# Performance work log

Measured on AMD Instinct MI355X. Metric: run time of the kernel, lower is better.

Reference implementation:

```python
import jax, jax.numpy as jnp
import numpy as np

B, S, D, K = 16, 4096, 64, 4096

def setup_inputs() -> dict:
    key = jax.random.key(0)
    k1, k2 = jax.random.split(key)
    z = jax.random.normal(k1, (B, S, D), dtype=jnp.float32)
    # codebook initialized uniform(-1/K, 1/K) as in the torch module
    emb = jax.random.uniform(k2, (K, D), dtype=jnp.float32, minval=-1.0 / K, maxval=1.0 / K)
    return {"z": z, "emb": emb}

def reference(z, emb):
    Dm = emb.shape[1]
    flat_z = z.reshape(-1, Dm)                     # [N, D]
    # squared L2 distances to every codebook entry: [N, K]
    dist = (jnp.sum(flat_z * flat_z, axis=1, keepdims=True)
            + jnp.sum(emb * emb, axis=1)
            - 2.0 * flat_z @ emb.T)
    encoding_indices = jnp.argmin(dist, axis=1)    # [N]
    # one-hot @ emb is mathematically a gather; use the direct gather
    quantized = emb[encoding_indices].reshape(z.shape)
    quantized_st = z + jax.lax.stop_gradient(quantized - z)
    e_latent_loss = jnp.mean((jax.lax.stop_gradient(quantized) - z) ** 2)
    q_latent_loss = jnp.mean((quantized - jax.lax.stop_gradient(z)) ** 2)
    vq_loss = e_latent_loss + q_latent_loss
    return quantized_st, encoding_indices.reshape(z.shape[:-1]), vq_loss
```

## Files before the change

kernel.cpp:

```cpp
#include <hip/hip_runtime.h>

#define NTOK 65536
#define DDIM 64
#define KCB  4096
#define MB   64
#define NTILES 256
#define TPW  64
#define LCAP 6144
#define WWIN 5.0e-4f
#define IDXOFF  (NTOK * DDIM)
#define LOSSOFF (NTOK * DDIM + NTOK)
#define ZPAD 68

typedef __bf16 bf16x8 __attribute__((ext_vector_type(8)));
typedef float  f32x4  __attribute__((ext_vector_type(4)));

__device__ __forceinline__ float opaque(float x) { asm volatile("" : "+v"(x)); return x; }

__device__ __forceinline__ float np_sumsq64(const float* __restrict__ v) {
    float r[8];
#pragma unroll
    for (int j = 0; j < 8; ++j) r[j] = opaque(v[j] * v[j]);
#pragma unroll
    for (int i = 1; i < 8; ++i)
#pragma unroll
        for (int j = 0; j < 8; ++j) r[j] += opaque(v[8 * i + j] * v[8 * i + j]);
    return ((r[0] + r[1]) + (r[2] + r[3])) + ((r[4] + r[5]) + (r[6] + r[7]));
}

__device__ __forceinline__ unsigned short bf16rne(float x) {
    unsigned u = __float_as_uint(x);
    return (unsigned short)((u + 0x7fffu + ((u >> 16) & 1u)) >> 16);
}

__global__ void k_prep(const float* __restrict__ emb, float* __restrict__ e2,
                       uint4* __restrict__ pfh, double* __restrict__ lossacc) {
    int k = blockIdx.x * blockDim.x + threadIdx.x;
    if (k == 0) *lossacc = 0.0;
    if (k >= KCB) return;
    float row[DDIM];
    const float4* r4 = (const float4*)(emb + (size_t)k * DDIM);
#pragma unroll
    for (int i = 0; i < DDIM / 4; ++i) {
        float4 v = r4[i];
        row[4*i+0] = v.x; row[4*i+1] = v.y; row[4*i+2] = v.z; row[4*i+3] = v.w;
    }
    e2[k] = np_sumsq64(row);
    const int tile = k >> 4, rr = k & 15;
#pragma unroll
    for (int q = 0; q < 4; ++q) {
#pragma unroll
        for (int kh = 0; kh < 2; ++kh) {
            union { uint4 v; unsigned short s[8]; } th;
#pragma unroll
            for (int j = 0; j < 8; ++j) th.s[j] = bf16rne(row[q*8 + kh*32 + j]);
            pfh[(size_t)tile * 128 + kh * 64 + q * 16 + rr] = th.v;
        }
    }
}

__global__ __launch_bounds__(256, 4)
void k_vq(const float* __restrict__ z, const float* __restrict__ emb,
          const float* __restrict__ e2g, const uint4* __restrict__ pfh,
          float* __restrict__ out, double* __restrict__ lossacc) {
    __shared__ float z2s[MB];
    __shared__ unsigned v0u[MB];
    __shared__ unsigned long long keys[MB];
    __shared__ unsigned list[LCAP];
    __shared__ int lcnt;
    __shared__ int bidx_s[MB];
    __shared__ float zrow_s[MB][ZPAD];

    const int tid  = threadIdx.x;
    const int lane = tid & 63;
    const int l15  = lane & 15;
    const int quad = lane >> 4;
    const int wn   = tid >> 6;
    const int tok0 = blockIdx.x * MB;
    const size_t zbase = (size_t)tok0 * DDIM;

    if (tid < MB) { v0u[tid] = 0x7f800000u; keys[tid] = 0xFFFFFFFFFFFFFFFFull; }
    if (tid == 0) lcnt = 0;

    bf16x8 Ah[4][2];
#pragma unroll
    for (int ms = 0; ms < 4; ++ms) {
        const float* p = z + zbase + (size_t)(ms * 16 + l15) * DDIM + quad * 8;
#pragma unroll
        for (int kh = 0; kh < 2; ++kh) {
            float4 u0 = *(const float4*)(p + kh * 32);
            float4 u1 = *(const float4*)(p + kh * 32 + 4);
            float d[8] = {-(u0.x + u0.x), -(u0.y + u0.y), -(u0.z + u0.z), -(u0.w + u0.w),
                          -(u1.x + u1.x), -(u1.y + u1.y), -(u1.z + u1.z), -(u1.w + u1.w)};
            union { bf16x8 v; unsigned short u[8]; } th;
#pragma unroll
            for (int j = 0; j < 8; ++j) th.u[j] = bf16rne(d[j]);
            Ah[ms][kh] = th.v;
        }
    }

#pragma unroll
    for (int it = 0; it < 4; ++it) {
        int f = it * 256 + tid;
        int tt = f >> 4, cc = f & 15;
        float4 v = ((const float4*)(z + zbase))[f];
        *(float4*)&zrow_s[tt][cc * 4] = v;
    }
    __syncthreads();

    if (tid < MB) {
        float row[DDIM];
#pragma unroll
        for (int i = 0; i < DDIM / 4; ++i) {
            float4 v = *(const float4*)&zrow_s[tid][i * 4];
            row[4*i+0] = v.x; row[4*i+1] = v.y; row[4*i+2] = v.z; row[4*i+3] = v.w;
        }
        z2s[tid] = np_sumsq64(row);
    }

    const uint4* pbase = pfh + (size_t)(wn * TPW) * 128 + lane;
    const int ncbase = (wn * TPW) * 16 + l15;

    float rm[16];
#pragma unroll
    for (int i = 0; i < 16; ++i) rm[i] = 3.0e38f;
#pragma unroll 1
    for (int t = 0; t < 8; ++t) {
        union { uint4 q; bf16x8 v; } b0, b1;
        b0.q = pbase[(size_t)t * 128]; b1.q = pbase[(size_t)t * 128 + 64];
#pragma unroll
        for (int ms = 0; ms < 4; ++ms) {
            f32x4 a = {0.5f, 0.5f, 0.5f, 0.5f};
            a = __builtin_amdgcn_mfma_f32_16x16x32_bf16(Ah[ms][0], b0.v, a, 0, 0, 0);
            a = __builtin_amdgcn_mfma_f32_16x16x32_bf16(Ah[ms][1], b1.v, a, 0, 0, 0);
#pragma unroll
            for (int r = 0; r < 4; ++r) rm[ms*4+r] = fminf(rm[ms*4+r], a[r]);
        }
    }
#pragma unroll
    for (int i = 0; i < 16; ++i) {
        float v = rm[i];
        v = fminf(v, __shfl_xor(v, 1));
        v = fminf(v, __shfl_xor(v, 2));
        v = fminf(v, __shfl_xor(v, 4));
        v = fminf(v, __shfl_xor(v, 8));
        if (l15 == 0)
            atomicMin(&v0u[(i >> 2) * 16 + quad * 4 + (i & 3)], __float_as_uint(v));
    }
    __syncthreads();

    float thr[16];
#pragma unroll
    for (int i = 0; i < 16; ++i)
        thr[i] = __uint_as_float(v0u[(i >> 2) * 16 + quad * 4 + (i & 3)]) + WWIN;

    auto compute2 = [&](uint4 p0, uint4 p1, uint4 q0, uint4 q1, int t) {
        unsigned mask = 0;
        {
            union { uint4 q; bf16x8 v; } b0, b1;
            b0.q = p0; b1.q = p1;
#pragma unroll
            for (int ms = 0; ms < 4; ++ms) {
                f32x4 a = {0.5f, 0.5f, 0.5f, 0.5f};
                a = __builtin_amdgcn_mfma_f32_16x16x32_bf16(Ah[ms][0], b0.v, a, 0, 0, 0);
                a = __builtin_amdgcn_mfma_f32_16x16x32_bf16(Ah[ms][1], b1.v, a, 0, 0, 0);
#pragma unroll
                for (int r = 0; r < 4; ++r) {
                    const int i = ms * 4 + r;
                    mask |= (a[r] <= thr[i]) ? (1u << i) : 0u;
                }
            }
        }
        {
            union { uint4 q; bf16x8 v; } b0, b1;
            b0.q = q0; b1.q = q1;
#pragma unroll
            for (int ms = 0; ms < 4; ++ms) {
                f32x4 a = {0.5f, 0.5f, 0.5f, 0.5f};
                a = __builtin_amdgcn_mfma_f32_16x16x32_bf16(Ah[ms][0], b0.v, a, 0, 0, 0);
                a = __builtin_amdgcn_mfma_f32_16x16x32_bf16(Ah[ms][1], b1.v, a, 0, 0, 0);
#pragma unroll
                for (int r = 0; r < 4; ++r) {
                    const int i = ms * 4 + r;
                    mask |= (a[r] <= thr[i]) ? (1u << (16 + i)) : 0u;
                }
            }
        }
        while (mask) {
            int b = __builtin_ctz(mask);
            mask &= mask - 1;
            int ts = b >> 4, i = b & 15;
            int m = (i >> 2) * 16 + quad * 4 + (i & 3);
            int ncol = ncbase + (t + ts) * 16;
            int idx = atomicAdd(&lcnt, 1);
            if (idx < LCAP)
                list[idx] = ((unsigned)m << 12) | (unsigned)ncol;
        }
    };

    uint4 a0 = pbase[0],   a1 = pbase[64];
    uint4 b0 = pbase[128], b1 = pbase[192];
    const uint4* pf = pbase + 256;
#pragma unroll 1
    for (int t = 0; t < TPW; t += 2) {
        uint4 c0 = a0, c1 = a1, d0 = b0, d1 = b1;
        if (t + 2 < TPW) {
            c0 = pf[0]; c1 = pf[64]; d0 = pf[128]; d1 = pf[192];
            pf += 256;
        }
        compute2(a0, a1, b0, b1, t);
        a0 = c0; a1 = c1; b0 = d0; b1 = d1;
    }
    __syncthreads();

    int cnt = lcnt; if (cnt > LCAP) cnt = LCAP;
    for (int i = tid; i < cnt; i += 256) {
        unsigned e = list[i];
        int m = (int)(e >> 12), n = (int)(e & 4095u);
        const float4* er4 = (const float4*)(emb + (size_t)n * DDIM);
        const float4* zr4 = (const float4*)&zrow_s[m][0];
        float a = 0.f;
#pragma unroll
        for (int j4 = 0; j4 < 16; ++j4) {
            float4 ev = er4[j4];
            float4 zv = zr4[j4];
            a = fmaf(zv.x + zv.x, ev.x, a);
            a = fmaf(zv.y + zv.y, ev.y, a);
            a = fmaf(zv.z + zv.z, ev.z, a);
            a = fmaf(zv.w + zv.w, ev.w, a);
        }
        float s = (z2s[m] + e2g[n]) - a;
        unsigned long long key = ((unsigned long long)__float_as_uint(s) << 32)
                               | (unsigned long long)(unsigned)n;
        atomicMin(&keys[m], key);
    }
    __syncthreads();

    if (tid < MB) {
        int nstar = (int)(keys[tid] & 0xffffffffULL);
        bidx_s[tid] = nstar;
        out[IDXOFF + tok0 + tid] = (float)nstar;
    }
    __syncthreads();

    float* red = (float*)list;
    float lsum = 0.f;
#pragma unroll
    for (int it = 0; it < 4; ++it) {
        int f  = it * 256 + tid;
        int tt = f >> 4, cc = f & 15;
        int idx = bidx_s[tt];
        float4 qv = ((const float4*)(emb + (size_t)idx * DDIM))[cc];
        float4 zv = *(const float4*)&zrow_s[tt][cc * 4];
        ((float4*)(out + zbase))[f] = qv;
        float dx = qv.x - zv.x, dy = qv.y - zv.y;
        float dz = qv.z - zv.z, dw = qv.w - zv.w;
        lsum += dx * dx + dy * dy + dz * dz + dw * dw;
    }
    red[tid] = lsum;
    __syncthreads();
    for (int s = 128; s > 0; s >>= 1) {
        if (tid < s) red[tid] += red[tid + s];
        __syncthreads();
    }
    if (tid == 0) atomicAdd(lossacc, (double)red[0]);
}

__global__ void k_fin(const double* __restrict__ lossacc, float* __restrict__ out) {
    out[LOSSOFF] = (float)(2.0 * (*lossacc) / (double)(NTOK * DDIM));
}

extern "C" void kernel_launch(void* const* d_in, const int* in_sizes, int n_in,
                              void* d_out, int out_size, void* d_ws, size_t ws_size,
                              hipStream_t stream) {
    const float* z   = (const float*)d_in[0];
    const float* emb = (const float*)d_in[1];
    float* out = (float*)d_out;

    char* ws = (char*)d_ws;
    float*  e2g     = (float*)(ws);
    uint4*  pfh     = (uint4*)(ws + 16384);
    double* lossacc = (double*)(ws + 16384 + 524288);

    hipLaunchKernelGGL(k_prep, dim3(64), dim3(64), 0, stream, emb, e2g, pfh, lossacc);
    hipLaunchKernelGGL(k_vq, dim3(NTOK / MB), dim3(256), 0, stream,
                       z, emb, e2g, pfh, out, lossacc);
    hipLaunchKernelGGL(k_fin, dim3(1), dim3(1), 0, stream, lossacc, out);
}
```

Before: 168.7 us.

## Split waves over token halves and codebook halves; add exact fallback on list overflow

```diff
diff --git a/kernel.cpp b/kernel.cpp
--- a/kernel.cpp
+++ b/kernel.cpp
@@ -5,8 +5,8 @@
 #define KCB  4096
 #define MB   64
 #define NTILES 256
-#define TPW  64
-#define LCAP 6144
+#define TPW  128
+#define LCAP 4096
 #define WWIN 5.0e-4f
 #define IDXOFF  (NTOK * DDIM)
 #define LOSSOFF (NTOK * DDIM + NTOK)
@@ -76,16 +76,18 @@
     const int l15  = lane & 15;
     const int quad = lane >> 4;
     const int wn   = tid >> 6;
+    const int g    = wn >> 1;
+    const int hh   = wn & 1;
     const int tok0 = blockIdx.x * MB;
     const size_t zbase = (size_t)tok0 * DDIM;
 
     if (tid < MB) { v0u[tid] = 0x7f800000u; keys[tid] = 0xFFFFFFFFFFFFFFFFull; }
     if (tid == 0) lcnt = 0;
 
-    bf16x8 Ah[4][2];
-#pragma unroll
-    for (int ms = 0; ms < 4; ++ms) {
-        const float* p = z + zbase + (size_t)(ms * 16 + l15) * DDIM + quad * 8;
+    bf16x8 Ah[2][2];
+#pragma unroll
+    for (int ms = 0; ms < 2; ++ms) {
+        const float* p = z + zbase + (size_t)((2 * g + ms) * 16 + l15) * DDIM + quad * 8;
 #pragma unroll
         for (int kh = 0; kh < 2; ++kh) {
             float4 u0 = *(const float4*)(p + kh * 32);
@@ -118,18 +120,18 @@
         z2s[tid] = np_sumsq64(row);
     }
 
-    const uint4* pbase = pfh + (size_t)(wn * TPW) * 128 + lane;
-    const int ncbase = (wn * TPW) * 16 + l15;
-
-    float rm[16];
-#pragma unroll
-    for (int i = 0; i < 16; ++i) rm[i] = 3.0e38f;
+    const uint4* pbase = pfh + (size_t)hh * 128 * 128 + lane;
+    const int ncbase = hh * 128 * 16 + l15;
+
+    float rm[8];
+#pragma unroll
+    for (int i = 0; i < 8; ++i) rm[i] = 3.0e38f;
 #pragma unroll 1
-    for (int t = 0; t < 8; ++t) {
+    for (int t = 0; t < 16; ++t) {
         union { uint4 q; bf16x8 v; } b0, b1;
         b0.q = pbase[(size_t)t * 128]; b1.q = pbase[(size_t)t * 128 + 64];
 #pragma unroll
-        for (int ms = 0; ms < 4; ++ms) {
+        for (int ms = 0; ms < 2; ++ms) {
             f32x4 a = {0.5f, 0.5f, 0.5f, 0.5f};
             a = __builtin_amdgcn_mfma_f32_16x16x32_bf16(Ah[ms][0], b0.v, a, 0, 0, 0);
             a = __builtin_amdgcn_mfma_f32_16x16x32_bf16(Ah[ms][1], b1.v, a, 0, 0, 0);
@@ -138,21 +140,21 @@
         }
     }
 #pragma unroll
-    for (int i = 0; i < 16; ++i) {
+    for (int i = 0; i < 8; ++i) {
         float v = rm[i];
         v = fminf(v, __shfl_xor(v, 1));
         v = fminf(v, __shfl_xor(v, 2));
         v = fminf(v, __shfl_xor(v, 4));
         v = fminf(v, __shfl_xor(v, 8));
         if (l15 == 0)
-            atomicMin(&v0u[(i >> 2) * 16 + quad * 4 + (i & 3)], __float_as_uint(v));
-    }
-    __syncthreads();
-
-    float thr[16];
-#pragma unroll
-    for (int i = 0; i < 16; ++i)
-        thr[i] = __uint_as_float(v0u[(i >> 2) * 16 + quad * 4 + (i & 3)]) + WWIN;
+            atomicMin(&v0u[(2*g + (i>>2)) * 16 + quad*4 + (i&3)], __float_as_uint(v));
+    }
+    __syncthreads();
+
+    float thr[8];
+#pragma unroll
+    for (int i = 0; i < 8; ++i)
+        thr[i] = __uint_as_float(v0u[(2*g + (i>>2)) * 16 + quad*4 + (i&3)]) + WWIN;
 
     auto compute2 = [&](uint4 p0, uint4 p1, uint4 q0, uint4 q1, int t) {
         unsigned mask = 0;
@@ -160,37 +162,33 @@
             union { uint4 q; bf16x8 v; } b0, b1;
             b0.q = p0; b1.q = p1;
 #pragma unroll
-            for (int ms = 0; ms < 4; ++ms) {
+            for (int ms = 0; ms < 2; ++ms) {
                 f32x4 a = {0.5f, 0.5f, 0.5f, 0.5f};
                 a = __builtin_amdgcn_mfma_f32_16x16x32_bf16(Ah[ms][0], b0.v, a, 0, 0, 0);
                 a = __builtin_amdgcn_mfma_f32_16x16x32_bf16(Ah[ms][1], b1.v, a, 0, 0, 0);
 #pragma unroll
-                for (int r = 0; r < 4; ++r) {
-                    const int i = ms * 4 + r;
-                    mask |= (a[r] <= thr[i]) ? (1u << i) : 0u;
-                }
+                for (int r = 0; r < 4; ++r)
+                    mask |= (a[r] <= thr[ms*4+r]) ? (1u << (ms*4+r)) : 0u;
             }
         }
         {
             union { uint4 q; bf16x8 v; } b0, b1;
             b0.q = q0; b1.q = q1;
 #pragma unroll
-            for (int ms = 0; ms < 4; ++ms) {
+            for (int ms = 0; ms < 2; ++ms) {
                 f32x4 a = {0.5f, 0.5f, 0.5f, 0.5f};
                 a = __builtin_amdgcn_mfma_f32_16x16x32_bf16(Ah[ms][0], b0.v, a, 0, 0, 0);
                 a = __builtin_amdgcn_mfma_f32_16x16x32_bf16(Ah[ms][1], b1.v, a, 0, 0, 0);
 #pragma unroll
-                for (int r = 0; r < 4; ++r) {
-                    const int i = ms * 4 + r;
-                    mask |= (a[r] <= thr[i]) ? (1u << (16 + i)) : 0u;
-                }
+                for (int r = 0; r < 4; ++r)
+                    mask |= (a[r] <= thr[ms*4+r]) ? (1u << (8 + ms*4+r)) : 0u;
             }
         }
         while (mask) {
             int b = __builtin_ctz(mask);
             mask &= mask - 1;
-            int ts = b >> 4, i = b & 15;
-            int m = (i >> 2) * 16 + quad * 4 + (i & 3);
+            int ts = b >> 3, i = b & 7;
+            int m = (2*g + (i >> 2)) * 16 + quad * 4 + (i & 3);
             int ncol = ncbase + (t + ts) * 16;
             int idx = atomicAdd(&lcnt, 1);
             if (idx < LCAP)
@@ -213,26 +211,48 @@
     }
     __syncthreads();
 
-    int cnt = lcnt; if (cnt > LCAP) cnt = LCAP;
-    for (int i = tid; i < cnt; i += 256) {
-        unsigned e = list[i];
-        int m = (int)(e >> 12), n = (int)(e & 4095u);
-        const float4* er4 = (const float4*)(emb + (size_t)n * DDIM);
-        const float4* zr4 = (const float4*)&zrow_s[m][0];
-        float a = 0.f;
-#pragma unroll
-        for (int j4 = 0; j4 < 16; ++j4) {
-            float4 ev = er4[j4];
-            float4 zv = zr4[j4];
-            a = fmaf(zv.x + zv.x, ev.x, a);
-            a = fmaf(zv.y + zv.y, ev.y, a);
-            a = fmaf(zv.z + zv.z, ev.z, a);
-            a = fmaf(zv.w + zv.w, ev.w, a);
-        }
-        float s = (z2s[m] + e2g[n]) - a;
-        unsigned long long key = ((unsigned long long)__float_as_uint(s) << 32)
-                               | (unsigned long long)(unsigned)n;
-        atomicMin(&keys[m], key);
+    int cnt = lcnt;
+    if (cnt <= LCAP) {
+        for (int i = tid; i < cnt; i += 256) {
+            unsigned e = list[i];
+            int m = (int)(e >> 12), n = (int)(e & 4095u);
+            const float4* er4 = (const float4*)(emb + (size_t)n * DDIM);
+            const float4* zr4 = (const float4*)&zrow_s[m][0];
+            float a = 0.f;
+#pragma unroll
+            for (int j4 = 0; j4 < 16; ++j4) {
+                float4 ev = er4[j4];
+                float4 zv = zr4[j4];
+                a = fmaf(zv.x + zv.x, ev.x, a);
+                a = fmaf(zv.y + zv.y, ev.y, a);
+                a = fmaf(zv.z + zv.z, ev.z, a);
+                a = fmaf(zv.w + zv.w, ev.w, a);
+            }
+            float s = (z2s[m] + e2g[n]) - a;
+            unsigned long long key = ((unsigned long long)__float_as_uint(s) << 32)
+                                   | (unsigned long long)(unsigned)n;
+            atomicMin(&keys[m], key);
+        }
+    } else {
+        for (int i = tid; i < MB * KCB; i += 256) {
+            int m = i >> 12, n = i & 4095;
+            const float4* er4 = (const float4*)(emb + (size_t)n * DDIM);
+            const float4* zr4 = (const float4*)&zrow_s[m][0];
+            float a = 0.f;
+#pragma unroll
+            for (int j4 = 0; j4 < 16; ++j4) {
+                float4 ev = er4[j4];
+                float4 zv = zr4[j4];
+                a = fmaf(zv.x + zv.x, ev.x, a);
+                a = fmaf(zv.y + zv.y, ev.y, a);
+                a = fmaf(zv.z + zv.z, ev.z, a);
+                a = fmaf(zv.w + zv.w, ev.w, a);
+            }
+            float s = (z2s[m] + e2g[n]) - a;
+            unsigned long long key = ((unsigned long long)__float_as_uint(s) << 32)
+                                   | (unsigned long long)(unsigned)n;
+            atomicMin(&keys[m], key);
+        }
     }
     __syncthreads();
 
```

Measured after the change: 156.6 us. 1.08x faster.
